# Performance work log

Measured on AMD Instinct MI355X. Metric: run time of the kernel, lower is better.

Reference implementation:

```python
import jax, jax.numpy as jnp
import numpy as np

B, D, N, H, K = 4, 1024, 4096, 16, 128
DH = D // H  # per-head dim (note: torch view splits D as (DH, H) in that order)
BN_EPS = 1e-3


def conv1(x, w, b):
    # 1x1 Conv1d == channel matmul: x [B,Cin,N], w [Cout,Cin], b [Cout]
    return jnp.einsum('oi,bin->bon', w, x) + b[None, :, None]


def setup_inputs() -> dict:
    key = jax.random.key(0)
    ks = jax.random.split(key, 16)
    s = 0.02
    proj_std = 1.0 / np.sqrt(K)  # init_() uniform(-1/sqrt(k), 1/sqrt(k))
    return {
        'x': jax.random.normal(ks[0], (B, D, N), jnp.float32),
        'source': jax.random.normal(ks[1], (B, D, N), jnp.float32),
        'to_q_w': jax.random.normal(ks[2], (D, D), jnp.float32) * s,
        'to_q_b': jnp.zeros((D,), jnp.float32),
        'to_k_w': jax.random.normal(ks[3], (D, D), jnp.float32) * s,
        'to_k_b': jnp.zeros((D,), jnp.float32),
        'proj_k': jax.random.uniform(ks[4], (N, K), jnp.float32, -proj_std, proj_std),
        'merge_w': jax.random.normal(ks[5], (D, D), jnp.float32) * s,
        'merge_b': jnp.zeros((D,), jnp.float32),
        'mlp_w1': jax.random.normal(ks[6], (2 * D, 2 * D), jnp.float32) * s,
        'mlp_b1': jnp.zeros((2 * D,), jnp.float32),
        'bn_gamma': jnp.ones((2 * D,), jnp.float32),
        'bn_beta': jnp.zeros((2 * D,), jnp.float32),
        'bn_mean': jnp.zeros((2 * D,), jnp.float32),
        'bn_var': jnp.ones((2 * D,), jnp.float32),
        'mlp_w2': jax.random.normal(ks[7], (D, 2 * D), jnp.float32) * s,
        'mlp_b2': jnp.zeros((D,), jnp.float32),
    }


def reference(x, source, to_q_w, to_q_b, to_k_w, to_k_b, proj_k, merge_w, merge_b,
              mlp_w1, mlp_b1, bn_gamma, bn_beta, bn_mean, bn_var, mlp_w2, mlp_b2):
    b = x.shape[0]
    q = conv1(x, to_q_w, to_q_b)          # [B,D,N]
    k = conv1(source, to_k_w, to_k_b)     # [B,D,M]
    v = k                                  # share_kv=True
    # Linformer sequence-length reduction: M -> K (proj_v == proj_k when shared)
    k = jnp.einsum('bdm,mk->bdk', k, proj_k)   # [B,D,K]
    v = jnp.einsum('bdm,mk->bdk', v, proj_k)   # [B,D,K]
    # torch .view(B, dim, heads, -1): channel axis split as (DH, H)
    qh = q.reshape(b, DH, H, N)
    kh = k.reshape(b, DH, H, K)
    vh = v.reshape(b, DH, H, K)
    scores = jnp.einsum('bdhn,bdhk->bhnk', qh, kh) / (DH ** 0.5)
    prob = jax.nn.softmax(scores, axis=-1)      # [B,H,N,K], small K
    msg = jnp.einsum('bhnk,bdhk->bdhn', prob, vh).reshape(b, D, N)
    msg = conv1(msg, merge_w, merge_b)
    # MLP([2D, 2D, D]): conv -> BN(eval, eps=1e-3) -> ReLU -> conv
    h = jnp.concatenate([x, msg], axis=1)       # [B,2D,N]
    h = conv1(h, mlp_w1, mlp_b1)
    h = bn_gamma[None, :, None] * (h - bn_mean[None, :, None]) \
        * jax.lax.rsqrt(bn_var + BN_EPS)[None, :, None] + bn_beta[None, :, None]
    h = jax.nn.relu(h)
    return conv1(h, mlp_w2, mlp_b2)             # [B,D,N]
```

## Files before the change

### kernel.cpp

```cpp
#include <hip/hip_runtime.h>
#include <stdint.h>

typedef __bf16 bf16x8 __attribute__((ext_vector_type(8)));
typedef float f32x4 __attribute__((ext_vector_type(4)));

__device__ __forceinline__ unsigned short f2bf(float f) {
    union { float f; uint32_t i; } v;
    v.f = f;
    uint32_t x = v.i;
    return (unsigned short)((x + 0x7FFFu + ((x >> 16) & 1u)) >> 16);
}

typedef __attribute__((address_space(3))) unsigned int lds_u32;
typedef __attribute__((address_space(1))) const unsigned int glob_u32;
__device__ __forceinline__ void gld16(const unsigned short* g, unsigned short* l) {
    __builtin_amdgcn_global_load_lds((glob_u32*)g, (lds_u32*)l, 16, 0, 0);
}

__global__ __launch_bounds__(256) void prep_weights(
    const float* __restrict__ Wq, const float* __restrict__ Wk,
    const float* __restrict__ Wm, const float* __restrict__ W1,
    const float* __restrict__ W2, const float* __restrict__ bq,
    const float* __restrict__ bk,
    unsigned short* __restrict__ wqb, unsigned short* __restrict__ wkb,
    unsigned short* __restrict__ wmb, unsigned short* __restrict__ w1b,
    unsigned short* __restrict__ w2b, float* __restrict__ bqp,
    float* __restrict__ bkp)
{
    const int b = blockIdx.x, t = threadIdx.x;
    if (b < 2048) {
        const float* in = (b < 1024) ? Wq : Wk;
        unsigned short* out = (b < 1024) ? wqb : wkb;
        const int i = ((b & 1023) * 256 + t) * 4;
        const int row = i >> 10, col = i & 1023;
        const float4 v = *(const float4*)(in + ((row & 63) * 16 + (row >> 6)) * 1024 + col);
        out[i + 0] = f2bf(v.x); out[i + 1] = f2bf(v.y);
        out[i + 2] = f2bf(v.z); out[i + 3] = f2bf(v.w);
    } else if (b < 3072) {
        const int i = ((b - 2048) * 256 + t) * 4;
        const int row = i >> 10, c0 = i & 1023;
        const float* r = Wm + (size_t)row * 1024;
#pragma unroll
        for (int j = 0; j < 4; ++j) {
            const int c = c0 + j;
            wmb[i + j] = f2bf(r[(c & 63) * 16 + (c >> 6)]);
        }
    } else if (b < 7168) {
        const int i = ((b - 3072) * 256 + t) * 4;
        const float4 v = *(const float4*)(W1 + i);
        w1b[i + 0] = f2bf(v.x); w1b[i + 1] = f2bf(v.y);
        w1b[i + 2] = f2bf(v.z); w1b[i + 3] = f2bf(v.w);
    } else if (b < 9216) {
        const int i = ((b - 7168) * 256 + t) * 4;
        const float4 v = *(const float4*)(W2 + i);
        w2b[i + 0] = f2bf(v.x); w2b[i + 1] = f2bf(v.y);
        w2b[i + 2] = f2bf(v.z); w2b[i + 3] = f2bf(v.w);
    } else {
        const int o = (b - 9216) * 256 + t;
        const int src = (o & 63) * 16 + (o >> 6);
        bqp[o] = bq[src];
        bkp[o] = bk[src];
    }
}

__global__ __launch_bounds__(256) void cvt_transpose(
    const float* __restrict__ in, unsigned short* __restrict__ out,
    int R, int C)
{
    __shared__ unsigned short tile[32][33];
    const size_t bo = (size_t)blockIdx.z * R * C;
    const int c0 = blockIdx.x * 32, r0 = blockIdx.y * 32;
    const int tx = threadIdx.x & 31, ty = threadIdx.x >> 5;
#pragma unroll
    for (int i = 0; i < 4; ++i)
        tile[ty + i * 8][tx] = f2bf(in[bo + (size_t)(r0 + ty + i * 8) * C + (c0 + tx)]);
    __syncthreads();
#pragma unroll
    for (int i = 0; i < 4; ++i)
        out[bo + (size_t)(c0 + ty + i * 8) * R + (r0 + tx)] = tile[tx][ty + i * 8];
}

__global__ __launch_bounds__(256) void cvt_transpose_xs(
    const float* __restrict__ x, const float* __restrict__ s,
    unsigned short* __restrict__ xt, unsigned short* __restrict__ st)
{
    __shared__ unsigned short tile[32][33];
    const int z = blockIdx.z;
    const float* in = (z < 4) ? x : s;
    unsigned short* out = (z < 4) ? xt : st;
    const size_t bo = (size_t)(z & 3) * 1024 * 4096;
    const int c0 = blockIdx.x * 32, r0 = blockIdx.y * 32;
    const int tx = threadIdx.x & 31, ty = threadIdx.x >> 5;
#pragma unroll
    for (int i = 0; i < 4; ++i)
        tile[ty + i * 8][tx] = f2bf(in[bo + (size_t)(r0 + ty + i * 8) * 4096 + (c0 + tx)]);
    __syncthreads();
#pragma unroll
    for (int i = 0; i < 4; ++i)
        out[bo + (size_t)(c0 + ty + i * 8) * 1024 + (r0 + tx)] = tile[tx][ty + i * 8];
}

template<int LDA, int LDB, int LDC, int KD, int SPLIT, bool CONCAT>
__global__ __launch_bounds__(256) void gemm_bt(
    const unsigned short* __restrict__ A,
    const unsigned short* __restrict__ A2, int K1,
    const unsigned short* __restrict__ BT,
    unsigned short* __restrict__ C, float* __restrict__ Cf,
    long long strideA, long long strideB, long long strideC,
    const float* __restrict__ bias_m,
    const float* __restrict__ bias_n,
    const float* __restrict__ bn_g,
    const float* __restrict__ bn_b,
    const float* __restrict__ bn_mu,
    const float* __restrict__ bn_var)
{
    constexpr int KPB = KD / SPLIT;
    __shared__ __align__(16) unsigned short As[128 * 64];
    __shared__ __align__(16) unsigned short Bs[128 * 64];

    const int z = blockIdx.z;
    const int batch = z / SPLIT;
    const int kbase = (z % SPLIT) * KPB;
    const int m0 = blockIdx.y * 128, n0 = blockIdx.x * 128;
    const unsigned short* Ab  = A + (size_t)batch * strideA;
    const unsigned short* A2b = CONCAT ? A2 + (size_t)batch * strideA
                                       : (const unsigned short*)0;
    const unsigned short* Bb = BT + (size_t)batch * strideB;

    const int t = threadIdx.x;
    const int lane = t & 63, wid = t >> 6;
    const int wm = wid >> 1, wn = wid & 1;
    const int r16 = lane & 15, quad = lane >> 4;

    f32x4 acc[4][4];
    const f32x4 zf = {0.f, 0.f, 0.f, 0.f};
#pragma unroll
    for (int i = 0; i < 4; ++i)
#pragma unroll
        for (int j = 0; j < 4; ++j) acc[i][j] = zf;

    for (int kt = kbase; kt < kbase + KPB; kt += 64) {
        const unsigned short* Asrc = Ab;
        int kk = kt;
        if (CONCAT && kt >= K1) { Asrc = A2b; kk = kt - K1; }
#pragma unroll
        for (int i = 0; i < 4; ++i) {
            const int p = i * 256 + t;
            const int row = p >> 3, slot = p & 7;
            const int kc = (slot ^ (row & 7)) * 8;
            gld16(&Asrc[(size_t)(m0 + row) * LDA + kk + kc], &As[p * 8]);
            gld16(&Bb[(size_t)(n0 + row) * LDB + kt + kc], &Bs[p * 8]);
        }
        __syncthreads();
#pragma unroll
        for (int s = 0; s < 2; ++s) {
            bf16x8 af[4], bfb[4];
#pragma unroll
            for (int i = 0; i < 4; ++i) {
                const int ra = wm * 64 + i * 16 + r16;
                const int rb = wn * 64 + i * 16 + r16;
                af[i]  = *(const bf16x8*)&As[(ra * 8 + ((s * 4 + quad) ^ (ra & 7))) * 8];
                bfb[i] = *(const bf16x8*)&Bs[(rb * 8 + ((s * 4 + quad) ^ (rb & 7))) * 8];
            }
#pragma unroll
            for (int mi = 0; mi < 4; ++mi)
#pragma unroll
                for (int ni = 0; ni < 4; ++ni)
                    acc[mi][ni] = __builtin_amdgcn_mfma_f32_16x16x32_bf16(
                        af[mi], bfb[ni], acc[mi][ni], 0, 0, 0);
        }
        __syncthreads();
    }

    unsigned short* Cb = C ? C + (size_t)z * strideC : (unsigned short*)0;
    float* Cfb = Cf ? Cf + (size_t)z * strideC : (float*)0;
    const bool has_bn = (bn_g != 0);
#pragma unroll
    for (int ni = 0; ni < 4; ++ni) {
        const int gn = n0 + wn * 64 + ni * 16 + r16;
        const float addn = bias_n ? bias_n[gn] : 0.f;
        float g = 1.f, bb = 0.f, mu = 0.f, rstd = 1.f;
        if (has_bn) {
            g = bn_g[gn]; bb = bn_b[gn]; mu = bn_mu[gn];
            rstd = rsqrtf(bn_var[gn] + 1e-3f);
        }
#pragma unroll
        for (int mi = 0; mi < 4; ++mi) {
            const int gm0 = m0 + wm * 64 + mi * 16 + quad * 4;
#pragma unroll
            for (int r = 0; r < 4; ++r) {
                float v = acc[mi][ni][r] + addn;
                if (bias_m) v += bias_m[gm0 + r];
                if (has_bn) { v = g * (v - mu) * rstd + bb; v = fmaxf(v, 0.f); }
                const size_t idx = (size_t)(gm0 + r) * LDC + gn;
                if (Cfb) Cfb[idx] = v;
                else     Cb[idx]  = f2bf(v);
            }
        }
    }
}

#define BAR   __builtin_amdgcn_s_barrier()
#define LGKM0 asm volatile("s_waitcnt lgkmcnt(0)" ::: "memory")
#define PRIO1 __builtin_amdgcn_s_setprio(1)
#define PRIO0 __builtin_amdgcn_s_setprio(0)

#define ST_A(dst, kt, i0, i1) do {                                          \
    const unsigned short* S_ = Ab; long long kk_ = (kt);                    \
    if (CONCAT && (kt) >= K1) { S_ = A2b; kk_ = (kt) - K1; }                \
    gld16(&S_[offA[i0] + kk_], (dst) + po[i0]);                             \
    gld16(&S_[offA[i1] + kk_], (dst) + po[i1]); } while (0)

#define ST_B(dst, kt, i0, i1) do {                                          \
    gld16(&Bb[offB[i0] + (kt)], (dst) + po[i0]);                            \
    gld16(&Bb[offB[i1] + (kt)], (dst) + po[i1]); } while (0)

#define RD_A(mh, AC) do {                                                   \
    _Pragma("unroll") for (int mi = 0; mi < 4; ++mi) {                      \
        const int ra = wm * 128 + (mh) * 64 + mi * 16 + r16;                \
        _Pragma("unroll") for (int ks = 0; ks < 2; ++ks) {                  \
            const int c_ = ks * 4 + quad;                                   \
            a[mi][ks] = *(const bf16x8*)&(AC)[(ra * 8 + (c_ ^ (ra & 7))) * 8]; \
        } } } while (0)

#define RD_B(np, BC) do {                                                   \
    _Pragma("unroll") for (int i = 0; i < 2; ++i) {                         \
        const int rb = wn * 64 + ((np) * 2 + i) * 16 + r16;                 \
        _Pragma("unroll") for (int ks = 0; ks < 2; ++ks) {                  \
            const int c_ = ks * 4 + quad;                                   \
            b[(np) * 2 + i][ks] = *(const bf16x8*)&(BC)[(rb * 8 + (c_ ^ (rb & 7))) * 8]; \
        } } } while (0)

#define MFMA_PH(mh, np) do {                                                \
    _Pragma("unroll") for (int mi = 0; mi < 4; ++mi)                        \
    _Pragma("unroll") for (int i = 0; i < 2; ++i)                           \
    _Pragma("unroll") for (int ks = 0; ks < 2; ++ks)                        \
        acc[(mh) * 4 + mi][(np) * 2 + i] =                                  \
            __builtin_amdgcn_mfma_f32_16x16x32_bf16(                        \
                a[mi][ks], b[(np) * 2 + i][ks],                             \
                acc[(mh) * 4 + mi][(np) * 2 + i], 0, 0, 0); } while (0)

#define TILE_BODY(XV, AC, BC, AN, BN_) do {                                 \
    const int kt1_ = ((XV) + 1) * 64;                                       \
    const bool g1_ = ((XV) + 1) < nt;                                       \
          \
    RD_A(0, AC); RD_B(0, BC); RD_B(1, BC);                                  \
    if (g1_) { ST_A(AN, kt1_, 0, 2); ST_B(BN_, kt1_, 0, 1);                 \
               ST_B(BN_, kt1_, 2, 3);                                       \
               asm volatile("s_waitcnt vmcnt(6)" ::: "memory"); }           \
    else     { asm volatile("s_waitcnt vmcnt(0)" ::: "memory"); }           \
    BAR; LGKM0; PRIO1; MFMA_PH(0, 0); MFMA_PH(0, 1); PRIO0; BAR;            \
                      \
    RD_A(1, AC);                                                            \
    if (g1_) { ST_A(AN, kt1_, 1, 3);                                        \
               asm volatile("s_waitcnt vmcnt(2)" ::: "memory"); }           \
    else     { asm volatile("s_waitcnt vmcnt(0)" ::: "memory"); }           \
    BAR; LGKM0; PRIO1; MFMA_PH(1, 1); MFMA_PH(1, 0); PRIO0; BAR;            \
} while (0)

template<int LDA, int LDB, int LDC, int KD, bool CONCAT>
__global__ __launch_bounds__(512, 2) void gemm256(
    const unsigned short* __restrict__ A,
    const unsigned short* __restrict__ A2, int K1,
    const unsigned short* __restrict__ BT,
    unsigned short* __restrict__ C, float* __restrict__ Cf,
    long long strideA, long long strideB, long long strideC,
    const float* __restrict__ bias_m,
    const float* __restrict__ bias_n,
    const float* __restrict__ bn_g,
    const float* __restrict__ bn_b,
    const float* __restrict__ bn_mu,
    const float* __restrict__ bn_var)
{
    static_assert(KD % 128 == 0, "nt must be even");
    constexpr int nt = KD / 64;
    constexpr int TILE = 256 * 64;
    __shared__ __align__(16) unsigned short As0[TILE];
    __shared__ __align__(16) unsigned short As1[TILE];
    __shared__ __align__(16) unsigned short Bs0[TILE];
    __shared__ __align__(16) unsigned short Bs1[TILE];

    const int batch = blockIdx.z;
    const int gx = gridDim.x;
    const int nwg = gx * gridDim.y;
    int flat = blockIdx.y * gx + blockIdx.x;
    flat = (flat & 7) * (nwg >> 3) + (flat >> 3);
    const int n0 = (flat % gx) * 256;
    const int m0 = (flat / gx) * 256;

    const unsigned short* Ab  = A + (size_t)batch * strideA;
    const unsigned short* A2b = CONCAT ? A2 + (size_t)batch * strideA
                                       : (const unsigned short*)0;
    const unsigned short* Bb  = BT + (size_t)batch * strideB;

    const int t = threadIdx.x;
    const int lane = t & 63, wid = t >> 6;
    const int wm = wid >> 2, wn = wid & 3;
    const int r16 = lane & 15, quad = lane >> 4;

    long long offA[4], offB[4];
    int po[4];
#pragma unroll
    for (int i = 0; i < 4; ++i) {
        const int p = i * 512 + t, row = p >> 3;
        const int kc = ((p & 7) ^ (row & 7)) * 8;
        po[i] = p * 8;
        offA[i] = (long long)(m0 + row) * LDA + kc;
        offB[i] = (long long)(n0 + row) * LDB + kc;
    }

    f32x4 acc[8][4];
    const f32x4 zf = {0.f, 0.f, 0.f, 0.f};
#pragma unroll
    for (int i = 0; i < 8; ++i)
#pragma unroll
        for (int j = 0; j < 4; ++j) acc[i][j] = zf;

    bf16x8 a[4][2], b[4][2];

    ST_A(As0, 0, 0, 2);
    ST_B(Bs0, 0, 0, 1);
    ST_B(Bs0, 0, 2, 3);
    ST_A(As0, 0, 1, 3);
    asm volatile("s_waitcnt vmcnt(2)" ::: "memory");
    BAR;

#pragma unroll 1
    for (int X2 = 0; X2 < nt; X2 += 2) {
        TILE_BODY(X2,     As0, Bs0, As1, Bs1);
        TILE_BODY(X2 + 1, As1, Bs1, As0, Bs0);
    }

    unsigned short* Cb = C ? C + (size_t)batch * strideC : (unsigned short*)0;
    float* Cfb = Cf ? Cf + (size_t)batch * strideC : (float*)0;
    const bool has_bn = (bn_g != 0);

    float addn4[4], g4[4], b4[4], mu4[4], rs4[4];
#pragma unroll
    for (int ni = 0; ni < 4; ++ni) {
        const int gn = n0 + wn * 64 + ni * 16 + r16;
        addn4[ni] = bias_n ? bias_n[gn] : 0.f;
        if (has_bn) {
            g4[ni] = bn_g[gn]; b4[ni] = bn_b[gn]; mu4[ni] = bn_mu[gn];
            rs4[ni] = rsqrtf(bn_var[gn] + 1e-3f);
        }
    }
#pragma unroll
    for (int mi = 0; mi < 8; ++mi) {
        const int gm0 = m0 + wm * 128 + mi * 16 + quad * 4;
#pragma unroll
        for (int r = 0; r < 4; ++r) {
            const float bm_ = bias_m ? bias_m[gm0 + r] : 0.f;
            const size_t rowb = (size_t)(gm0 + r) * LDC + n0 + wn * 64 + r16;
#pragma unroll
            for (int ni = 0; ni < 4; ++ni) {
                float v = acc[mi][ni][r] + addn4[ni] + bm_;
                if (has_bn) {
                    v = g4[ni] * (v - mu4[ni]) * rs4[ni] + b4[ni];
                    v = fmaxf(v, 0.f);
                }
                if (Cfb) Cfb[rowb + ni * 16] = v;
                else     Cb[rowb + ni * 16]  = f2bf(v);
            }
        }
    }
}

#undef TILE_BODY
#undef MFMA_PH
#undef RD_B
#undef RD_A
#undef ST_B
#undef ST_A
#undef PRIO0
#undef PRIO1
#undef LGKM0
#undef BAR

__global__ __launch_bounds__(256) void reduce_kp(
    const float* __restrict__ acc, unsigned short* __restrict__ kpb)
{
    const int j = (blockIdx.x * 256 + threadIdx.x) * 4;
    const int b = j >> 17, jj = j & 131071;
    const float* base = acc + (size_t)b * 8 * 131072 + jj;
    float4 s = *(const float4*)base;
#pragma unroll
    for (int p = 1; p < 8; ++p) {
        const float4 v = *(const float4*)(base + (size_t)p * 131072);
        s.x += v.x; s.y += v.y; s.z += v.z; s.w += v.w;
    }
    kpb[j + 0] = f2bf(s.x); kpb[j + 1] = f2bf(s.y);
    kpb[j + 2] = f2bf(s.z); kpb[j + 3] = f2bf(s.w);
}

__global__ __launch_bounds__(256) void attn_fused(
    const unsigned short* __restrict__ qT,
    const unsigned short* __restrict__ kp,
    unsigned short* __restrict__ msgT)
{
    constexpr int QS = 72, KS = 72, VS = 136, PS = 136;
    __shared__ __align__(16) unsigned short QKP[128 * QS + 128 * KS];
    __shared__ __align__(16) unsigned short Vs[64 * VS];
    unsigned short* Qs = QKP;
    unsigned short* Ks = QKP + 128 * QS;
    unsigned short* Ps = QKP;

    const int t = threadIdx.x;
    const int lane = t & 63, w = t >> 6;
    const int r16 = lane & 15, quad = lane >> 4;
    const int h = blockIdx.y, n0 = blockIdx.x * 128;
    const size_t b = blockIdx.z;

    const unsigned short* qbase = qT + (b * 4096 + n0) * 1024 + h * 64;
    const unsigned short* kbase = kp + (b * 1024 + h * 64) * 128;

#pragma unroll
    for (int i = 0; i < 4; ++i) {
        const int c = i * 256 + t;
        const int n = c >> 3, dh0 = (c & 7) * 8;
        *(int4*)&Qs[n * QS + dh0] = *(const int4*)&qbase[(size_t)n * 1024 + dh0];
    }
#pragma unroll
    for (int i = 0; i < 4; ++i) {
        const int c = i * 256 + t;
        const int kkq = c & 3, dh = (c >> 2) & 63, kkh = c >> 8;
        const int kk0 = kkh * 32 + kkq * 8;
        const bf16x8 v = *(const bf16x8*)&kbase[(size_t)dh * 128 + kk0];
        *(bf16x8*)&Vs[dh * VS + kk0] = v;
        const unsigned short* vs = (const unsigned short*)&v;
#pragma unroll
        for (int j = 0; j < 8; ++j) Ks[(kk0 + j) * KS + dh] = vs[j];
    }
    __syncthreads();

    f32x4 S[2][8];
    const f32x4 zf = {0.f, 0.f, 0.f, 0.f};
#pragma unroll
    for (int mi = 0; mi < 2; ++mi)
#pragma unroll
        for (int ni = 0; ni < 8; ++ni) S[mi][ni] = zf;

    bf16x8 aq[2][2];
#pragma unroll
    for (int mi = 0; mi < 2; ++mi)
#pragma unroll
        for (int ks = 0; ks < 2; ++ks)
            aq[mi][ks] = *(const bf16x8*)&Qs[(w * 32 + mi * 16 + r16) * QS + ks * 32 + quad * 8];
#pragma unroll
    for (int ni = 0; ni < 8; ++ni) {
        const bf16x8 b0 = *(const bf16x8*)&Ks[(ni * 16 + r16) * KS + quad * 8];
        const bf16x8 b1 = *(const bf16x8*)&Ks[(ni * 16 + r16) * KS + 32 + quad * 8];
#pragma unroll
        for (int mi = 0; mi < 2; ++mi) {
            S[mi][ni] = __builtin_amdgcn_mfma_f32_16x16x32_bf16(aq[mi][0], b0, S[mi][ni], 0, 0, 0);
            S[mi][ni] = __builtin_amdgcn_mfma_f32_16x16x32_bf16(aq[mi][1], b1, S[mi][ni], 0, 0, 0);
        }
    }

    __syncthreads();

    float linv[2][4];
#pragma unroll
    for (int mi = 0; mi < 2; ++mi) {
        float e[8][4];
        float rs0 = 0.f, rs1 = 0.f, rs2 = 0.f, rs3 = 0.f;
#pragma unroll
        for (int ni = 0; ni < 8; ++ni) {
            e[ni][0] = __expf(S[mi][ni][0] * 0.125f); rs0 += e[ni][0];
            e[ni][1] = __expf(S[mi][ni][1] * 0.125f); rs1 += e[ni][1];
            e[ni][2] = __expf(S[mi][ni][2] * 0.125f); rs2 += e[ni][2];
            e[ni][3] = __expf(S[mi][ni][3] * 0.125f); rs3 += e[ni][3];
        }
        float rs[4] = {rs0, rs1, rs2, rs3};
#pragma unroll
        for (int r = 0; r < 4; ++r) {
            float s = rs[r];
            s += __shfl_xor(s, 1); s += __shfl_xor(s, 2);
            s += __shfl_xor(s, 4); s += __shfl_xor(s, 8);
            linv[mi][r] = 1.f / s;
        }
#pragma unroll
        for (int ni = 0; ni < 8; ++ni)
#pragma unroll
            for (int r = 0; r < 4; ++r)
                Ps[(w * 32 + mi * 16 + quad * 4 + r) * PS + ni * 16 + r16] = f2bf(e[ni][r]);
    }
    __syncthreads();

    f32x4 O[2][4];
#pragma unroll
    for (int mi = 0; mi < 2; ++mi)
#pragma unroll
        for (int ni = 0; ni < 4; ++ni) O[mi][ni] = zf;

    bf16x8 ap[2][4];
#pragma unroll
    for (int mi = 0; mi < 2; ++mi)
#pragma unroll
        for (int ks = 0; ks < 4; ++ks)
            ap[mi][ks] = *(const bf16x8*)&Ps[(w * 32 + mi * 16 + r16) * PS + ks * 32 + quad * 8];
#pragma unroll
    for (int ni = 0; ni < 4; ++ni)
#pragma unroll
        for (int ks = 0; ks < 4; ++ks) {
            const bf16x8 bv = *(const bf16x8*)&Vs[(ni * 16 + r16) * VS + ks * 32 + quad * 8];
#pragma unroll
            for (int mi = 0; mi < 2; ++mi)
                O[mi][ni] = __builtin_amdgcn_mfma_f32_16x16x32_bf16(ap[mi][ks], bv, O[mi][ni], 0, 0, 0);
        }

    unsigned short* ob = msgT + (b * 4096 + n0) * 1024 + h * 64;
#pragma unroll
    for (int mi = 0; mi < 2; ++mi)
#pragma unroll
        for (int ni = 0; ni < 4; ++ni)
#pragma unroll
            for (int r = 0; r < 4; ++r)
                ob[(size_t)(w * 32 + mi * 16 + quad * 4 + r) * 1024 + ni * 16 + r16] =
                    f2bf(O[mi][ni][r] * linv[mi][r]);
}

extern "C" void kernel_launch(void* const* d_in, const int* in_sizes, int n_in,
                              void* d_out, int out_size, void* d_ws, size_t ws_size,
                              hipStream_t stream)
{
    (void)in_sizes; (void)n_in; (void)out_size; (void)ws_size;
    const float* x    = (const float*)d_in[0];
    const float* srcp = (const float*)d_in[1];
    const float* Wq   = (const float*)d_in[2];
    const float* bq   = (const float*)d_in[3];
    const float* Wk   = (const float*)d_in[4];
    const float* bk   = (const float*)d_in[5];
    const float* proj = (const float*)d_in[6];
    const float* Wm   = (const float*)d_in[7];
    const float* bm   = (const float*)d_in[8];
    const float* W1   = (const float*)d_in[9];
    const float* b1   = (const float*)d_in[10];
    const float* gam  = (const float*)d_in[11];
    const float* bet  = (const float*)d_in[12];
    const float* mu   = (const float*)d_in[13];
    const float* var  = (const float*)d_in[14];
    const float* W2   = (const float*)d_in[15];
    const float* b2   = (const float*)d_in[16];
    float* out = (float*)d_out;
    unsigned short* ws = (unsigned short*)d_ws;

    const long long E = 16777216LL;
    unsigned short* xt  = ws;
    unsigned short* st  = xt + E;
    unsigned short* qt  = st + E;
    unsigned short* kc  = qt + E;
    unsigned short* ht  = kc + E;
    unsigned short* pT  = ht + 2 * E;
    unsigned short* kpb = pT + 524288;
    unsigned short* wqb = kpb + 524288;
    unsigned short* wkb = wqb + 1048576;
    unsigned short* wmb = wkb + 1048576;
    unsigned short* w1b = wmb + 1048576;
    unsigned short* w2b = w1b + 4194304;
    float* bqp = (float*)(w2b + 2097152);
    float* bkp = bqp + 1024;
    float* kpacc = (float*)ht;

    cvt_transpose_xs<<<dim3(128, 32, 8), 256, 0, stream>>>(x, srcp, xt, st);
    cvt_transpose<<<dim3(4, 128, 1), 256, 0, stream>>>(proj, pT, 4096, 128);
    prep_weights<<<9220, 256, 0, stream>>>(Wq, Wk, Wm, W1, W2, bq, bk,
                                           wqb, wkb, wmb, w1b, w2b, bqp, bkp);

    gemm256<1024, 1024, 1024, 1024, false><<<dim3(4, 16, 4), 512, 0, stream>>>(
        xt, nullptr, 1024, wqb, qt, nullptr,
        4096LL * 1024, 0LL, 4096LL * 1024, nullptr, bqp,
        nullptr, nullptr, nullptr, nullptr);
    gemm256<1024, 1024, 4096, 1024, false><<<dim3(16, 4, 4), 512, 0, stream>>>(
        wkb, nullptr, 1024, st, kc, nullptr,
        0LL, 4096LL * 1024, 1024LL * 4096, bkp, nullptr,
        nullptr, nullptr, nullptr, nullptr);
    gemm_bt<4096, 4096, 128, 4096, 8, false><<<dim3(1, 8, 32), 256, 0, stream>>>(
        kc, nullptr, 4096, pT, nullptr, kpacc,
        1024LL * 4096, 0LL, 1024LL * 128, nullptr, nullptr,
        nullptr, nullptr, nullptr, nullptr);
    reduce_kp<<<512, 256, 0, stream>>>(kpacc, kpb);
    attn_fused<<<dim3(32, 16, 4), 256, 0, stream>>>(qt, kpb, qt);
    gemm256<1024, 1024, 1024, 1024, false><<<dim3(4, 16, 4), 512, 0, stream>>>(
        qt, nullptr, 1024, wmb, st, nullptr,
        4096LL * 1024, 0LL, 4096LL * 1024, nullptr, bm,
        nullptr, nullptr, nullptr, nullptr);
    gemm256<1024, 2048, 2048, 2048, true><<<dim3(8, 16, 4), 512, 0, stream>>>(
        xt, st, 1024, w1b, ht, nullptr,
        4096LL * 1024, 0LL, 4096LL * 2048, nullptr, b1,
        gam, bet, mu, var);
    gemm256<2048, 2048, 4096, 2048, false><<<dim3(16, 4, 4), 512, 0, stream>>>(
        w2b, nullptr, 2048, ht, nullptr, out,
        0LL, 4096LL * 2048, 1024LL * 4096, b2, nullptr,
        nullptr, nullptr, nullptr, nullptr);
}
```

Before: 618.4 us.

## Restructure gemm256 main loop with inline-asm LDS reads and two-tile prefetch

The 256x256 GEMM main loop is rewritten. Each 64-wide K tile is now consumed in two 32-wide halves, each using 12 ds_read_b128 loads issued through inline asm with precomputed swizzled LDS addresses, followed by 32 MFMAs. Global-to-LDS prefetch now runs two tiles ahead, issuing all loads for a buffer at once and waiting with vmcnt(8), and the four LDS buffers are merged into one array so immediate offsets can be used. The aim is to cut address arithmetic and scheduler-inserted waits and to overlap loads better, at the cost of more barriers and of correctness depending on the hand-computed offsets and wait counts.

```diff
diff --git a/kernel.cpp b/kernel.cpp
--- a/kernel.cpp
+++ b/kernel.cpp
@@ -15,6 +15,11 @@
 typedef __attribute__((address_space(1))) const unsigned int glob_u32;
 __device__ __forceinline__ void gld16(const unsigned short* g, unsigned short* l) {
     __builtin_amdgcn_global_load_lds((glob_u32*)g, (lds_u32*)l, 16, 0, 0);
+}
+
+typedef __attribute__((address_space(3))) unsigned short lds_us;
+__device__ __forceinline__ unsigned ldsaddr(unsigned short* p) {
+    return (unsigned)(uintptr_t)(lds_us*)p;
 }
 
 __global__ __launch_bounds__(256) void prep_weights(
@@ -202,8 +207,11 @@
 
 #define BAR   __builtin_amdgcn_s_barrier()
 #define LGKM0 asm volatile("s_waitcnt lgkmcnt(0)" ::: "memory")
+#define SB0   __builtin_amdgcn_sched_barrier(0)
 #define PRIO1 __builtin_amdgcn_s_setprio(1)
 #define PRIO0 __builtin_amdgcn_s_setprio(0)
+#define VMC8  asm volatile("s_waitcnt vmcnt(8)" ::: "memory")
+#define VMC0  asm volatile("s_waitcnt vmcnt(0)" ::: "memory")
 
 #define ST_A(dst, kt, i0, i1) do {                                          \
     const unsigned short* S_ = Ab; long long kk_ = (kt);                    \
@@ -215,47 +223,48 @@
     gld16(&Bb[offB[i0] + (kt)], (dst) + po[i0]);                            \
     gld16(&Bb[offB[i1] + (kt)], (dst) + po[i1]); } while (0)
 
-#define RD_A(mh, AC) do {                                                   \
-    _Pragma("unroll") for (int mi = 0; mi < 4; ++mi) {                      \
-        const int ra = wm * 128 + (mh) * 64 + mi * 16 + r16;                \
-        _Pragma("unroll") for (int ks = 0; ks < 2; ++ks) {                  \
-            const int c_ = ks * 4 + quad;                                   \
-            a[mi][ks] = *(const bf16x8*)&(AC)[(ra * 8 + (c_ ^ (ra & 7))) * 8]; \
-        } } } while (0)
-
-#define RD_B(np, BC) do {                                                   \
-    _Pragma("unroll") for (int i = 0; i < 2; ++i) {                         \
-        const int rb = wn * 64 + ((np) * 2 + i) * 16 + r16;                 \
-        _Pragma("unroll") for (int ks = 0; ks < 2; ++ks) {                  \
-            const int c_ = ks * 4 + quad;                                   \
-            b[(np) * 2 + i][ks] = *(const bf16x8*)&(BC)[(rb * 8 + (c_ ^ (rb & 7))) * 8]; \
-        } } } while (0)
-
-#define MFMA_PH(mh, np) do {                                                \
-    _Pragma("unroll") for (int mi = 0; mi < 4; ++mi)                        \
-    _Pragma("unroll") for (int i = 0; i < 2; ++i)                           \
-    _Pragma("unroll") for (int ks = 0; ks < 2; ++ks)                        \
-        acc[(mh) * 4 + mi][(np) * 2 + i] =                                  \
-            __builtin_amdgcn_mfma_f32_16x16x32_bf16(                        \
-                a[mi][ks], b[(np) * 2 + i][ks],                             \
-                acc[(mh) * 4 + mi][(np) * 2 + i], 0, 0, 0); } while (0)
-
-#define TILE_BODY(XV, AC, BC, AN, BN_) do {                                 \
-    const int kt1_ = ((XV) + 1) * 64;                                       \
-    const bool g1_ = ((XV) + 1) < nt;                                       \
-          \
-    RD_A(0, AC); RD_B(0, BC); RD_B(1, BC);                                  \
-    if (g1_) { ST_A(AN, kt1_, 0, 2); ST_B(BN_, kt1_, 0, 1);                 \
-               ST_B(BN_, kt1_, 2, 3);                                       \
-               asm volatile("s_waitcnt vmcnt(6)" ::: "memory"); }           \
-    else     { asm volatile("s_waitcnt vmcnt(0)" ::: "memory"); }           \
-    BAR; LGKM0; PRIO1; MFMA_PH(0, 0); MFMA_PH(0, 1); PRIO0; BAR;            \
-                      \
-    RD_A(1, AC);                                                            \
-    if (g1_) { ST_A(AN, kt1_, 1, 3);                                        \
-               asm volatile("s_waitcnt vmcnt(2)" ::: "memory"); }           \
-    else     { asm volatile("s_waitcnt vmcnt(0)" ::: "memory"); }           \
-    BAR; LGKM0; PRIO1; MFMA_PH(1, 1); MFMA_PH(1, 0); PRIO0; BAR;            \
+#define DSR(d, b_, imm)                                                     \
+    asm volatile("ds_read_b128 %0, %1 offset:" #imm                         \
+                 : "=v"(d) : "v"(b_) : "memory")
+
+#define RD12(AB, BB) do {                                                   \
+    DSR(f0, AB, 0);    DSR(f1, AB, 2048);                                   \
+    DSR(f2, AB, 4096); DSR(f3, AB, 6144);                                   \
+    DSR(f4, AB, 8192); DSR(f5, AB, 10240);                                  \
+    DSR(f6, AB, 12288); DSR(f7, AB, 14336);                                 \
+    DSR(g0, BB, 0);    DSR(g1, BB, 2048);                                   \
+    DSR(g2, BB, 4096); DSR(g3, BB, 6144); } while (0)
+
+#define MM(i, j, ff, gg)                                                    \
+    acc[i][j] = __builtin_amdgcn_mfma_f32_16x16x32_bf16(ff, gg, acc[i][j], 0, 0, 0)
+
+#define MFMA32 do {                                                         \
+    MM(0,0,f0,g0); MM(0,1,f0,g1); MM(0,2,f0,g2); MM(0,3,f0,g3);             \
+    MM(1,0,f1,g0); MM(1,1,f1,g1); MM(1,2,f1,g2); MM(1,3,f1,g3);             \
+    MM(2,0,f2,g0); MM(2,1,f2,g1); MM(2,2,f2,g2); MM(2,3,f2,g3);             \
+    MM(3,0,f3,g0); MM(3,1,f3,g1); MM(3,2,f3,g2); MM(3,3,f3,g3);             \
+    MM(4,0,f4,g0); MM(4,1,f4,g1); MM(4,2,f4,g2); MM(4,3,f4,g3);             \
+    MM(5,0,f5,g0); MM(5,1,f5,g1); MM(5,2,f5,g2); MM(5,3,f5,g3);             \
+    MM(6,0,f6,g0); MM(6,1,f6,g1); MM(6,2,f6,g2); MM(6,3,f6,g3);             \
+    MM(7,0,f7,g0); MM(7,1,f7,g1); MM(7,2,f7,g2); MM(7,3,f7,g3); } while (0)
+
+#define BODY_E(XV, AK, BK) do {                                             \
+    RD12(AK, BK);                                                           \
+    LGKM0; SB0; BAR;                                                        \
+    PRIO1; MFMA32; PRIO0;                                                   \
+} while (0)
+
+#define BODY_O(XV, AK, BK, AD, BD) do {                                     \
+    RD12(AK, BK);                                                           \
+    LGKM0; SB0; BAR;                                                        \
+    if ((XV) + 2 < nt) {                                                    \
+        const int kt2_ = ((XV) + 2) * 64;                                   \
+        ST_A(AD, kt2_, 0, 2); ST_A(AD, kt2_, 1, 3);                         \
+        ST_B(BD, kt2_, 0, 1); ST_B(BD, kt2_, 2, 3);                         \
+        VMC8;                                                               \
+    } else { VMC0; }                                                        \
+    SB0; BAR;                                                               \
+    PRIO1; MFMA32; PRIO0;                                                   \
 } while (0)
 
 template<int LDA, int LDB, int LDC, int KD, bool CONCAT>
@@ -275,10 +284,11 @@
     static_assert(KD % 128 == 0, "nt must be even");
     constexpr int nt = KD / 64;
     constexpr int TILE = 256 * 64;
-    __shared__ __align__(16) unsigned short As0[TILE];
-    __shared__ __align__(16) unsigned short As1[TILE];
-    __shared__ __align__(16) unsigned short Bs0[TILE];
-    __shared__ __align__(16) unsigned short Bs1[TILE];
+    __shared__ __align__(16) unsigned short Ls[4 * TILE];
+    unsigned short* A0 = Ls;
+    unsigned short* A1 = Ls + TILE;
+    unsigned short* B0 = Ls + 2 * TILE;
+    unsigned short* B1 = Ls + 3 * TILE;
 
     const int batch = blockIdx.z;
     const int gx = gridDim.x;
@@ -309,6 +319,16 @@
         offB[i] = (long long)(n0 + row) * LDB + kc;
     }
 
+    const unsigned lb = ldsaddr(Ls);
+    const unsigned x0 = (unsigned)((quad ^ (r16 & 7)) * 16);
+    const unsigned x1 = (unsigned)(((4 + quad) ^ (r16 & 7)) * 16);
+    const unsigned rowa = lb + (unsigned)((wm * 128 + r16) * 128);
+    const unsigned rowb = lb + 65536u + (unsigned)((wn * 64 + r16) * 128);
+    const unsigned a_k0_0 = rowa + x0,           a_k1_0 = rowa + x1;
+    const unsigned a_k0_1 = rowa + 32768u + x0,  a_k1_1 = rowa + 32768u + x1;
+    const unsigned b_k0_0 = rowb + x0,           b_k1_0 = rowb + x1;
+    const unsigned b_k0_1 = rowb + 32768u + x0,  b_k1_1 = rowb + 32768u + x1;
+
     f32x4 acc[8][4];
     const f32x4 zf = {0.f, 0.f, 0.f, 0.f};
 #pragma unroll
@@ -316,19 +336,20 @@
 #pragma unroll
         for (int j = 0; j < 4; ++j) acc[i][j] = zf;
 
-    bf16x8 a[4][2], b[4][2];
-
-    ST_A(As0, 0, 0, 2);
-    ST_B(Bs0, 0, 0, 1);
-    ST_B(Bs0, 0, 2, 3);
-    ST_A(As0, 0, 1, 3);
-    asm volatile("s_waitcnt vmcnt(2)" ::: "memory");
-    BAR;
+    bf16x8 f0, f1, f2, f3, f4, f5, f6, f7, g0, g1, g2, g3;
+
+    ST_A(A0, 0, 0, 2);  ST_A(A0, 0, 1, 3);
+    ST_B(B0, 0, 0, 1);  ST_B(B0, 0, 2, 3);
+    ST_A(A1, 64, 0, 2); ST_A(A1, 64, 1, 3);
+    ST_B(B1, 64, 0, 1); ST_B(B1, 64, 2, 3);
+    VMC8; SB0; BAR;
 
 #pragma unroll 1
     for (int X2 = 0; X2 < nt; X2 += 2) {
-        TILE_BODY(X2,     As0, Bs0, As1, Bs1);
-        TILE_BODY(X2 + 1, As1, Bs1, As0, Bs0);
+        BODY_E(X2,     a_k0_0, b_k0_0);
+        BODY_O(X2,     a_k1_0, b_k1_0, A0, B0);
+        BODY_E(X2 + 1, a_k0_1, b_k0_1);
+        BODY_O(X2 + 1, a_k1_1, b_k1_1, A1, B1);
     }
 
     unsigned short* Cb = C ? C + (size_t)batch * strideC : (unsigned short*)0;
@@ -351,7 +372,7 @@
 #pragma unroll
         for (int r = 0; r < 4; ++r) {
             const float bm_ = bias_m ? bias_m[gm0 + r] : 0.f;
-            const size_t rowb = (size_t)(gm0 + r) * LDC + n0 + wn * 64 + r16;
+            const size_t rowc = (size_t)(gm0 + r) * LDC + n0 + wn * 64 + r16;
 #pragma unroll
             for (int ni = 0; ni < 4; ++ni) {
                 float v = acc[mi][ni][r] + addn4[ni] + bm_;
@@ -359,21 +380,26 @@
                     v = g4[ni] * (v - mu4[ni]) * rs4[ni] + b4[ni];
                     v = fmaxf(v, 0.f);
                 }
-                if (Cfb) Cfb[rowb + ni * 16] = v;
-                else     Cb[rowb + ni * 16]  = f2bf(v);
+                if (Cfb) Cfb[rowc + ni * 16] = v;
+                else     Cb[rowc + ni * 16]  = f2bf(v);
             }
         }
     }
 }
 
-#undef TILE_BODY
-#undef MFMA_PH
-#undef RD_B
-#undef RD_A
+#undef BODY_O
+#undef BODY_E
+#undef MFMA32
+#undef MM
+#undef RD12
+#undef DSR
 #undef ST_B
 #undef ST_A
+#undef VMC0
+#undef VMC8
 #undef PRIO0
 #undef PRIO1
+#undef SB0
 #undef LGKM0
 #undef BAR
 
```

Result: slower. 1.161 ms (+87.7%).

## Reassociate key path: project source by proj_k before applying Wk

Applied to the files above, without the earlier changes.

Computes Wk·(source·proj_k) instead of (Wk·source)·proj_k. The full 1024x1024x4096-per-batch key convolution is replaced by a source-by-proj GEMM plus a small Wk GEMM on the reduced 1024x128 tensor. The bias is folded in analytically through bk times the column sums of proj_k, computed by a new colsum kernel. The source no longer needs a transpose, only a bf16 conversion. This removes roughly one large GEMM's worth of FLOPs, at the cost of extra small kernels and a different bf16 rounding order.

```diff
diff --git a/kernel.cpp b/kernel.cpp
--- a/kernel.cpp
+++ b/kernel.cpp
@@ -82,22 +82,52 @@
 
 __global__ __launch_bounds__(256) void cvt_transpose_xs(
     const float* __restrict__ x, const float* __restrict__ s,
-    unsigned short* __restrict__ xt, unsigned short* __restrict__ st)
+    unsigned short* __restrict__ xt, unsigned short* __restrict__ sb)
 {
     __shared__ unsigned short tile[32][33];
     const int z = blockIdx.z;
-    const float* in = (z < 4) ? x : s;
-    unsigned short* out = (z < 4) ? xt : st;
     const size_t bo = (size_t)(z & 3) * 1024 * 4096;
     const int c0 = blockIdx.x * 32, r0 = blockIdx.y * 32;
     const int tx = threadIdx.x & 31, ty = threadIdx.x >> 5;
+    if (z >= 4) {
+#pragma unroll
+        for (int i = 0; i < 4; ++i) {
+            const size_t idx = bo + (size_t)(r0 + ty + i * 8) * 4096 + (c0 + tx);
+            sb[idx] = f2bf(s[idx]);
+        }
+        return;
+    }
 #pragma unroll
     for (int i = 0; i < 4; ++i)
-        tile[ty + i * 8][tx] = f2bf(in[bo + (size_t)(r0 + ty + i * 8) * 4096 + (c0 + tx)]);
+        tile[ty + i * 8][tx] = f2bf(x[bo + (size_t)(r0 + ty + i * 8) * 4096 + (c0 + tx)]);
     __syncthreads();
 #pragma unroll
     for (int i = 0; i < 4; ++i)
-        out[bo + (size_t)(c0 + ty + i * 8) * 1024 + (r0 + tx)] = tile[tx][ty + i * 8];
+        xt[bo + (size_t)(c0 + ty + i * 8) * 1024 + (r0 + tx)] = tile[tx][ty + i * 8];
+}
+
+__global__ __launch_bounds__(256) void colsum_pT(
+    const unsigned short* __restrict__ pT, float* __restrict__ cs)
+{
+    __shared__ float red[4];
+    const int k = blockIdx.x, t = threadIdx.x;
+    const unsigned short* row = pT + (size_t)k * 4096;
+    float s = 0.f;
+#pragma unroll
+    for (int it = 0; it < 2; ++it) {
+        const int4 v = *(const int4*)&row[(t + it * 256) * 8];
+        const unsigned short* u = (const unsigned short*)&v;
+#pragma unroll
+        for (int j = 0; j < 8; ++j) {
+            union { uint32_t i; float f; } w; w.i = (uint32_t)u[j] << 16;
+            s += w.f;
+        }
+    }
+#pragma unroll
+    for (int o = 1; o < 64; o <<= 1) s += __shfl_xor(s, o);
+    if ((t & 63) == 0) red[t >> 6] = s;
+    __syncthreads();
+    if (t == 0) cs[k] = red[0] + red[1] + red[2] + red[3];
 }
 
 template<int LDA, int LDB, int LDC, int KD, int SPLIT, bool CONCAT>
@@ -391,6 +421,27 @@
     }
     kpb[j + 0] = f2bf(s.x); kpb[j + 1] = f2bf(s.y);
     kpb[j + 2] = f2bf(s.z); kpb[j + 3] = f2bf(s.w);
+}
+
+__global__ __launch_bounds__(256) void reduce_kp2(
+    const float* __restrict__ acc, const float* __restrict__ bkp,
+    const float* __restrict__ cs, unsigned short* __restrict__ out)
+{
+    const int j = (blockIdx.x * 256 + threadIdx.x) * 4;
+    const int b = j >> 17, jj = j & 131071;
+    const int o = jj >> 7, kq = jj & 127;
+    const float* base = acc + (size_t)b * 8 * 131072 + jj;
+    float4 s = *(const float4*)base;
+#pragma unroll
+    for (int p = 1; p < 8; ++p) {
+        const float4 v = *(const float4*)(base + (size_t)p * 131072);
+        s.x += v.x; s.y += v.y; s.z += v.z; s.w += v.w;
+    }
+    const float bm = bkp[o];
+    out[j + 0] = f2bf(s.x + bm * cs[kq + 0]);
+    out[j + 1] = f2bf(s.y + bm * cs[kq + 1]);
+    out[j + 2] = f2bf(s.z + bm * cs[kq + 2]);
+    out[j + 3] = f2bf(s.w + bm * cs[kq + 3]);
 }
 
 __global__ __launch_bounds__(256) void attn_fused(
@@ -547,46 +598,55 @@
 
     const long long E = 16777216LL;
     unsigned short* xt  = ws;
-    unsigned short* st  = xt + E;
-    unsigned short* qt  = st + E;
-    unsigned short* kc  = qt + E;
-    unsigned short* ht  = kc + E;
+    unsigned short* sb  = xt + E;
+    unsigned short* qt  = sb + E;
+    unsigned short* ks  = qt + E;
+    unsigned short* ht  = ks + E;
     unsigned short* pT  = ht + 2 * E;
-    unsigned short* kpb = pT + 524288;
-    unsigned short* wqb = kpb + 524288;
+    unsigned short* spb = pT + 524288;
+    unsigned short* wqb = spb + 524288;
     unsigned short* wkb = wqb + 1048576;
     unsigned short* wmb = wkb + 1048576;
     unsigned short* w1b = wmb + 1048576;
     unsigned short* w2b = w1b + 4194304;
     float* bqp = (float*)(w2b + 2097152);
     float* bkp = bqp + 1024;
-    float* kpacc = (float*)ht;
-
-    cvt_transpose_xs<<<dim3(128, 32, 8), 256, 0, stream>>>(x, srcp, xt, st);
+    float* kpacc  = (float*)ht;
+    float* kpacc2 = (float*)ks;
+    float* cs     = kpacc2 + 32 * 131072;
+    unsigned short* kpf = (unsigned short*)(cs + 128);
+
+    cvt_transpose_xs<<<dim3(128, 32, 8), 256, 0, stream>>>(x, srcp, xt, sb);
     cvt_transpose<<<dim3(4, 128, 1), 256, 0, stream>>>(proj, pT, 4096, 128);
     prep_weights<<<9220, 256, 0, stream>>>(Wq, Wk, Wm, W1, W2, bq, bk,
                                            wqb, wkb, wmb, w1b, w2b, bqp, bkp);
+    colsum_pT<<<128, 256, 0, stream>>>(pT, cs);
 
     gemm256<1024, 1024, 1024, 1024, false><<<dim3(4, 16, 4), 512, 0, stream>>>(
         xt, nullptr, 1024, wqb, qt, nullptr,
         4096LL * 1024, 0LL, 4096LL * 1024, nullptr, bqp,
         nullptr, nullptr, nullptr, nullptr);
-    gemm256<1024, 1024, 4096, 1024, false><<<dim3(16, 4, 4), 512, 0, stream>>>(
-        wkb, nullptr, 1024, st, kc, nullptr,
-        0LL, 4096LL * 1024, 1024LL * 4096, bkp, nullptr,
+
+    gemm_bt<4096, 4096, 1024, 4096, 8, false><<<dim3(8, 1, 32), 256, 0, stream>>>(
+        pT, nullptr, 4096, sb, nullptr, kpacc,
+        0LL, 1024LL * 4096, 131072LL, nullptr, nullptr,
         nullptr, nullptr, nullptr, nullptr);
-    gemm_bt<4096, 4096, 128, 4096, 8, false><<<dim3(1, 8, 32), 256, 0, stream>>>(
-        kc, nullptr, 4096, pT, nullptr, kpacc,
-        1024LL * 4096, 0LL, 1024LL * 128, nullptr, nullptr,
+    reduce_kp<<<512, 256, 0, stream>>>(kpacc, spb);
+
+    gemm_bt<1024, 1024, 128, 1024, 8, false><<<dim3(1, 8, 32), 256, 0, stream>>>(
+        wkb, nullptr, 1024, spb, nullptr, kpacc2,
+        0LL, 131072LL, 131072LL, nullptr, nullptr,
         nullptr, nullptr, nullptr, nullptr);
-    reduce_kp<<<512, 256, 0, stream>>>(kpacc, kpb);
-    attn_fused<<<dim3(32, 16, 4), 256, 0, stream>>>(qt, kpb, qt);
+    reduce_kp2<<<512, 256, 0, stream>>>(kpacc2, bkp, cs, kpf);
+
+    attn_fused<<<dim3(32, 16, 4), 256, 0, stream>>>(qt, kpf, qt);
+
     gemm256<1024, 1024, 1024, 1024, false><<<dim3(4, 16, 4), 512, 0, stream>>>(
-        qt, nullptr, 1024, wmb, st, nullptr,
+        qt, nullptr, 1024, wmb, sb, nullptr,
         4096LL * 1024, 0LL, 4096LL * 1024, nullptr, bm,
         nullptr, nullptr, nullptr, nullptr);
     gemm256<1024, 2048, 2048, 2048, true><<<dim3(8, 16, 4), 512, 0, stream>>>(
-        xt, st, 1024, w1b, ht, nullptr,
+        xt, sb, 1024, w1b, ht, nullptr,
         4096LL * 1024, 0LL, 4096LL * 2048, nullptr, b1,
         gam, bet, mu, var);
     gemm256<2048, 2048, 4096, 2048, false><<<dim3(16, 4, 4), 512, 0, stream>>>(
```

Result: faster. 593.7 us (-4.0%).
